# Kernel tuning notes

Hardware: AMD Instinct MI355X
Metric: run time of the kernel (lower is better)

Reference implementation:

```python
import jax, jax.numpy as jnp
import numpy as np

N = 50000   # nodes
E = 800000  # edges
D = 96      # feature dim


def setup_inputs() -> dict:
    key = jax.random.key(0)
    k1, k2, k3, k4 = jax.random.split(key, 4)
    scale = 1.0 / np.sqrt(D)
    return {
        "x": jax.random.normal(k1, (N, D), dtype=jnp.float32),
        "edge_index": jax.random.randint(k2, (2, E), 0, N, dtype=jnp.int64),
        "W1": jax.random.normal(k3, (D, D), dtype=jnp.float32) * scale,
        "b1": jnp.zeros((D,), dtype=jnp.float32),
        "W2": jax.random.normal(k4, (D, D), dtype=jnp.float32) * scale,
        "b2": jnp.zeros((D,), dtype=jnp.float32),
    }


def _gcn_conv(x, src, dst, W, b, n_nodes):
    # PyG GCNConv: linear transform, add self-loops, symmetric normalization,
    # scatter-add aggregation from src (row) to dst (col), then bias.
    h = x @ W  # [N, D_out]
    loops = jnp.arange(n_nodes, dtype=src.dtype)
    s = jnp.concatenate([src, loops])  # [E+N]
    d = jnp.concatenate([dst, loops])  # [E+N]
    deg = jax.ops.segment_sum(jnp.ones_like(d, dtype=h.dtype), d, num_segments=n_nodes)
    dinv = jnp.where(deg > 0, jax.lax.rsqrt(deg), 0.0)  # deg^-1/2, 0 for isolated
    norm = dinv[s] * dinv[d]  # [E+N]
    msg = norm[:, None] * h[s]  # gather + scale
    out = jax.ops.segment_sum(msg, d, num_segments=n_nodes)  # scatter-add
    return out + b


def reference(x, edge_index, W1, b1, W2, b2):
    src, dst = edge_index[0], edge_index[1]
    # dropout p=0.0 -> identity. ReLU after every layer (loop break never fires).
    h = _gcn_conv(x, src, dst, W1, b1, N)
    h = jax.nn.relu(h)
    h = _gcn_conv(h, src, dst, W2, b2, N)
    h = jax.nn.relu(h)
    return h
```

## Files before the change

kernel.cpp:

```cpp
#include <hip/hip_runtime.h>
#include <hip/hip_fp16.h>

#define NN 50000
#define EE 800000
#define DD 96

#define NBIN 196
#define CE   4096
#define CB   196
#define EPT2 16
#define DB   64



__global__ __launch_bounds__(256) void k_hist(const int* __restrict__ ei,
                                              int* __restrict__ histB) {
    __shared__ int hist[NBIN];
    int t = threadIdx.x;
    if (t < NBIN) hist[t] = 0;
    __syncthreads();
    int e0 = blockIdx.x * CE;
#pragma unroll
    for (int k = 0; k < EPT2; ++k) {
        int e = e0 + k * 256 + t;
        if (e < EE) atomicAdd(&hist[ei[EE + e] >> 8], 1);
    }
    __syncthreads();
    if (t < NBIN) histB[t * CB + blockIdx.x] = hist[t];
}


__global__ __launch_bounds__(256) void k_scan_bins(int* __restrict__ histB,
                                                   int* __restrict__ binTot) {
    __shared__ int sh[256];
    int t = threadIdx.x;
    int b = blockIdx.x;
    int v = (t < CB) ? histB[b * CB + t] : 0;
    sh[t] = v;
    __syncthreads();
    for (int off = 1; off < 256; off <<= 1) {
        int u = (t >= off) ? sh[t - off] : 0;
        __syncthreads();
        sh[t] += u;
        __syncthreads();
    }
    if (t < CB) histB[b * CB + t] = sh[t] - v;
    if (t == 255) binTot[b] = sh[255];
}


__global__ __launch_bounds__(256) void k_scan_tot(const int* __restrict__ binTot,
                                                  int* __restrict__ binbase) {
    __shared__ int sh[256];
    int t = threadIdx.x;
    int v = (t < NBIN) ? binTot[t] : 0;
    sh[t] = v;
    __syncthreads();
    for (int off = 1; off < 256; off <<= 1) {
        int u = (t >= off) ? sh[t - off] : 0;
        __syncthreads();
        sh[t] += u;
        __syncthreads();
    }
    if (t < NBIN) binbase[t] = sh[t] - v;
    if (t == 0) binbase[NBIN] = EE;
}


__global__ __launch_bounds__(64) void k_scan_tot64(const int* __restrict__ binTotD,
                                                   int* __restrict__ degBase) {
    __shared__ int sh[DB];
    int t = threadIdx.x;
    int v = binTotD[t];
    sh[t] = v;
    __syncthreads();
    for (int off = 1; off < DB; off <<= 1) {
        int u = (t >= off) ? sh[t - off] : 0;
        __syncthreads();
        sh[t] += u;
        __syncthreads();
    }
    degBase[t] = sh[t] - v;
}


__global__ __launch_bounds__(256) void k_scatter_bins(const int* __restrict__ ei,
                                                      const int* __restrict__ histB,
                                                      const int* __restrict__ binbase,
                                                      int* __restrict__ packed) {
    __shared__ int hist[NBIN];
    __shared__ int lofs[NBIN + 1];
    __shared__ int cur[NBIN];
    __shared__ int sstart[NBIN];
    __shared__ int buf[CE];
    __shared__ int sh[256];
    int t = threadIdx.x;
    int e0 = blockIdx.x * CE;
    int nE = min(CE, EE - e0);

    int s[EPT2], d[EPT2];
#pragma unroll
    for (int k = 0; k < EPT2; ++k) {
        int e = e0 + k * 256 + t;
        s[k] = (e < EE) ? ei[e] : 0;
        d[k] = (e < EE) ? ei[EE + e] : -1;
    }
    if (t < NBIN) hist[t] = 0;
    __syncthreads();
#pragma unroll
    for (int k = 0; k < EPT2; ++k)
        if (d[k] >= 0) atomicAdd(&hist[d[k] >> 8], 1);
    __syncthreads();
    int v = (t < NBIN) ? hist[t] : 0;
    sh[t] = v;
    __syncthreads();
    for (int off = 1; off < 256; off <<= 1) {
        int u = (t >= off) ? sh[t - off] : 0;
        __syncthreads();
        sh[t] += u;
        __syncthreads();
    }
    if (t < NBIN) { lofs[t] = sh[t] - v; cur[t] = sh[t] - v; }
    if (t == 0) lofs[NBIN] = nE;
    if (t < NBIN) sstart[t] = binbase[t] + histB[t * CB + blockIdx.x];
    __syncthreads();
#pragma unroll
    for (int k = 0; k < EPT2; ++k)
        if (d[k] >= 0) {
            int b = d[k] >> 8;
            int pos = atomicAdd(&cur[b], 1);
            buf[pos] = s[k] | ((d[k] & 0xFF) << 16);
        }
    __syncthreads();
    for (int i = t; i < nE; i += 256) {
        int blo = 0, bhi = NBIN;
        while (bhi - blo > 1) {
            int mid = (blo + bhi) >> 1;
            if (lofs[mid] <= i) blo = mid; else bhi = mid;
        }
        packed[sstart[blo] + (i - lofs[blo])] = buf[i];
    }
}


__global__ __launch_bounds__(256) void k_csr(const int* __restrict__ packed,
                                             const int* __restrict__ binbase,
                                             int* __restrict__ rp,
                                             float* __restrict__ dinv,
                                             int* __restrict__ col,
                                             const float* __restrict__ x,
                                             __half* __restrict__ xh,
                                             int* __restrict__ histD) {
    __shared__ int h256[256];
    __shared__ int cur[256];
    __shared__ int sh[256];
    __shared__ float sdinv[256];
    __shared__ int hd[DB];
    int t = threadIdx.x;
    int b = blockIdx.x;
    int base = binbase[b];
    int nE = binbase[b + 1] - base;

    h256[t] = 0;
    if (t < DB) hd[t] = 0;
    __syncthreads();
    for (int i = t; i < nE; i += 256)
        atomicAdd(&h256[(packed[base + i] >> 16) & 0xFF], 1);
    __syncthreads();
    int v = h256[t];
    sh[t] = v;
    __syncthreads();
    for (int off = 1; off < 256; off <<= 1) {
        int u = (t >= off) ? sh[t - off] : 0;
        __syncthreads();
        sh[t] += u;
        __syncthreads();
    }
    int ex = sh[t] - v;
    cur[t] = ex;
    float di = rsqrtf((float)(v + 1));
    sdinv[t] = di;
    int node = b * 256 + t;
    if (node <= NN) rp[node] = base + ex;
    if (node < NN) {
        dinv[node] = di;
        atomicAdd(&hd[(DB - 1) - min(v, DB - 1)], 1);
    }
    __syncthreads();
    if (t < DB) histD[t * CB + b] = hd[t];
    for (int i = t; i < nE; i += 256) {
        int pv = packed[base + i];
        int pos = atomicAdd(&cur[(pv >> 16) & 0xFF], 1);
        col[base + pos] = pv & 0xFFFF;
    }
    for (int i = t; i < 256 * 12; i += 256) {
        int rr = i / 12;
        int cc = i % 12;
        int r = b * 256 + rr;
        if (r < NN) {
            float sc = sdinv[rr];
            const float4* xx = (const float4*)x + (size_t)r * 24 + cc * 2;
            float4 f0 = xx[0], f1 = xx[1];
            __half h[8];
            h[0] = __float2half_rn(sc * f0.x); h[1] = __float2half_rn(sc * f0.y);
            h[2] = __float2half_rn(sc * f0.z); h[3] = __float2half_rn(sc * f0.w);
            h[4] = __float2half_rn(sc * f1.x); h[5] = __float2half_rn(sc * f1.y);
            h[6] = __float2half_rn(sc * f1.z); h[7] = __float2half_rn(sc * f1.w);
            ((uint4*)xh)[(size_t)r * 12 + cc] = *(uint4*)h;
        }
    }
}


__global__ __launch_bounds__(256) void k_perm(const int* __restrict__ rp,
                                              const int* __restrict__ histD,
                                              const int* __restrict__ degBase,
                                              int* __restrict__ perm) {
    __shared__ int lcur[DB];
    int t = threadIdx.x;
    int b = blockIdx.x;
    if (t < DB) lcur[t] = 0;
    __syncthreads();
    int node = b * 256 + t;
    if (node < NN) {
        int deg = rp[node + 1] - rp[node];
        int bin = (DB - 1) - min(deg, DB - 1);
        int loc = atomicAdd(&lcur[bin], 1);
        perm[degBase[bin] + histD[bin * CB + b] + loc] = node;
    }
}


template <int FINAL>
__global__ __launch_bounds__(384) void k_fused(const __half* __restrict__ xh,
                                               const int* __restrict__ rp,
                                               const int* __restrict__ col,
                                               const float* __restrict__ dinv,
                                               const int* __restrict__ perm,
                                               const float* __restrict__ W,
                                               const float* __restrict__ b,
                                               __half* __restrict__ acth,
                                               float* __restrict__ outf) {
    __shared__ __half Wl[DD * DD];
    __shared__ float Al[32][100];
    int t = threadIdx.x;
    for (int i = t; i < DD * DD / 8; i += 384) {
        const float4* ww = (const float4*)W;
        float4 f0 = ww[i * 2], f1 = ww[i * 2 + 1];
        __half h[8];
        h[0] = __float2half_rn(f0.x); h[1] = __float2half_rn(f0.y);
        h[2] = __float2half_rn(f0.z); h[3] = __float2half_rn(f0.w);
        h[4] = __float2half_rn(f1.x); h[5] = __float2half_rn(f1.y);
        h[6] = __float2half_rn(f1.z); h[7] = __float2half_rn(f1.w);
        ((uint4*)Wl)[i] = *(uint4*)h;
    }

    int c  = t % 12;
    int ny = t / 12;
    int idx = blockIdx.x * 32 + ny;
    int d = (idx < NN) ? perm[idx] : NN;
    const uint4* h4 = (const uint4*)xh;

    if (d < NN) {
        union U { uint4 u; __half2 h[4]; };
        U self; self.u = h4[d * 12 + c];
        float dd = dinv[d];
        int j0 = rp[d], j1 = rp[d + 1];

        float2 aA[4] = {{0,0},{0,0},{0,0},{0,0}};
        float2 aB[4] = {{0,0},{0,0},{0,0},{0,0}};
        int j = j0;
        for (; j + 3 < j1; j += 4) {
            int s0 = col[j], s1 = col[j+1], s2 = col[j+2], s3 = col[j+3];
            U v0, v1, v2, v3;
            v0.u = h4[s0 * 12 + c];
            v1.u = h4[s1 * 12 + c];
            v2.u = h4[s2 * 12 + c];
            v3.u = h4[s3 * 12 + c];
#pragma unroll
            for (int k = 0; k < 4; ++k) {
                float2 f0 = __half22float2(v0.h[k]);
                float2 f1 = __half22float2(v1.h[k]);
                float2 f2 = __half22float2(v2.h[k]);
                float2 f3 = __half22float2(v3.h[k]);
                aA[k].x += f0.x + f1.x; aA[k].y += f0.y + f1.y;
                aB[k].x += f2.x + f3.x; aB[k].y += f2.y + f3.y;
            }
        }
        for (; j < j1; ++j) {
            U v; v.u = h4[col[j] * 12 + c];
#pragma unroll
            for (int k = 0; k < 4; ++k) {
                float2 f = __half22float2(v.h[k]);
                aA[k].x += f.x; aA[k].y += f.y;
            }
        }
        float v[8];
#pragma unroll
        for (int k = 0; k < 4; ++k) {
            float2 fs = __half22float2(self.h[k]);
            v[2*k]   = dd * (aA[k].x + aB[k].x + fs.x);
            v[2*k+1] = dd * (aA[k].y + aB[k].y + fs.y);
        }
        *(float4*)&Al[ny][c * 8]     = make_float4(v[0], v[1], v[2], v[3]);
        *(float4*)&Al[ny][c * 8 + 4] = make_float4(v[4], v[5], v[6], v[7]);
    }
    __syncthreads();

    int tx = t % 24;
    int ry = t / 24;
    int c0 = tx * 4;
    float a0x = 0.f, a0y = 0.f, a0z = 0.f, a0w = 0.f;
    float a1x = 0.f, a1y = 0.f, a1z = 0.f, a1w = 0.f;
#pragma unroll 8
    for (int k = 0; k < DD; ++k) {
        uint2 wv = *(const uint2*)&Wl[k * DD + c0];
        const __half2* wh = (const __half2*)&wv;
        float2 w01 = __half22float2(wh[0]);
        float2 w23 = __half22float2(wh[1]);
        float r0 = Al[ry][k];
        float r1 = Al[ry + 16][k];
        a0x += r0 * w01.x; a0y += r0 * w01.y; a0z += r0 * w23.x; a0w += r0 * w23.y;
        a1x += r1 * w01.x; a1y += r1 * w01.y; a1z += r1 * w23.x; a1w += r1 * w23.y;
    }
    float4 bb = *(const float4*)&b[c0];
    int i0 = blockIdx.x * 32 + ry;
    int i1 = i0 + 16;
    int g0 = (i0 < NN) ? perm[i0] : NN;
    int g1 = (i1 < NN) ? perm[i1] : NN;
    float r0x = fmaxf(a0x + bb.x, 0.f), r0y = fmaxf(a0y + bb.y, 0.f);
    float r0z = fmaxf(a0z + bb.z, 0.f), r0w = fmaxf(a0w + bb.w, 0.f);
    float r1x = fmaxf(a1x + bb.x, 0.f), r1y = fmaxf(a1y + bb.y, 0.f);
    float r1z = fmaxf(a1z + bb.z, 0.f), r1w = fmaxf(a1w + bb.w, 0.f);
    if (g0 < NN) {
        if (FINAL) {
            *(float4*)&outf[g0 * DD + c0] = make_float4(r0x, r0y, r0z, r0w);
        } else {
            float sc = dinv[g0];
            __half h[4];
            h[0] = __float2half_rn(sc * r0x); h[1] = __float2half_rn(sc * r0y);
            h[2] = __float2half_rn(sc * r0z); h[3] = __float2half_rn(sc * r0w);
            *(uint2*)&acth[g0 * DD + c0] = *(uint2*)h;
        }
    }
    if (g1 < NN) {
        if (FINAL) {
            *(float4*)&outf[g1 * DD + c0] = make_float4(r1x, r1y, r1z, r1w);
        } else {
            float sc = dinv[g1];
            __half h[4];
            h[0] = __float2half_rn(sc * r1x); h[1] = __float2half_rn(sc * r1y);
            h[2] = __float2half_rn(sc * r1z); h[3] = __float2half_rn(sc * r1w);
            *(uint2*)&acth[g1 * DD + c0] = *(uint2*)h;
        }
    }
}


extern "C" void kernel_launch(void* const* d_in, const int* in_sizes, int n_in,
                              void* d_out, int out_size, void* d_ws, size_t ws_size,
                              hipStream_t stream) {
    const float* x  = (const float*)d_in[0];
    const int*   ei = (const int*)d_in[1];
    const float* W1 = (const float*)d_in[2];
    const float* b1 = (const float*)d_in[3];
    const float* W2 = (const float*)d_in[4];
    const float* b2 = (const float*)d_in[5];
    float* out = (float*)d_out;

    char* p = (char*)d_ws;
    int*   histB   = (int*)p;   p += ((size_t)NBIN * CB * 4 + 255) & ~(size_t)255;
    int*   binTot  = (int*)p;   p += ((size_t)NBIN * 4 + 255) & ~(size_t)255;
    int*   binbase = (int*)p;   p += ((size_t)(NBIN + 1) * 4 + 255) & ~(size_t)255;
    int*   rp      = (int*)p;   p += ((size_t)(NN + 1) * 4 + 255) & ~(size_t)255;
    float* dinv    = (float*)p; p += ((size_t)NN * 4 + 255) & ~(size_t)255;
    int*   col     = (int*)p;   p += ((size_t)EE * 4 + 255) & ~(size_t)255;
    int*   histD   = (int*)p;   p += ((size_t)DB * CB * 4 + 255) & ~(size_t)255;
    int*   binTotD = (int*)p;   p += ((size_t)DB * 4 + 255) & ~(size_t)255;
    int*   degBase = (int*)p;   p += ((size_t)DB * 4 + 255) & ~(size_t)255;
    int*   perm    = (int*)p;   p += ((size_t)NN * 4 + 255) & ~(size_t)255;
    __half* bufA   = (__half*)p; p += ((size_t)NN * DD * 2 + 255) & ~(size_t)255;
    __half* bufB   = (__half*)p;
    int*   packed  = (int*)bufB;

    k_hist<<<CB, 256, 0, stream>>>(ei, histB);
    k_scan_bins<<<NBIN, 256, 0, stream>>>(histB, binTot);
    k_scan_tot<<<1, 256, 0, stream>>>(binTot, binbase);
    k_scatter_bins<<<CB, 256, 0, stream>>>(ei, histB, binbase, packed);
    k_csr<<<NBIN, 256, 0, stream>>>(packed, binbase, rp, dinv, col, x, bufA, histD);
    k_scan_bins<<<DB, 256, 0, stream>>>(histD, binTotD);
    k_scan_tot64<<<1, 64, 0, stream>>>(binTotD, degBase);
    k_perm<<<NBIN, 256, 0, stream>>>(rp, histD, degBase, perm);

    k_fused<0><<<(NN + 31) / 32, 384, 0, stream>>>(bufA, rp, col, dinv, perm,
                                                   W1, b1, bufB, nullptr);

    k_fused<1><<<(NN + 31) / 32, 384, 0, stream>>>(bufB, rp, col, dinv, perm,
                                                   W2, b2, nullptr, out);
}
```

Before: 137.4 us.

## Fold bin scans into consumers and build a block-local degree permutation inside k_csr

The two single-block scan kernels are removed. Each block of k_scatter_bins and k_csr now recomputes the exclusive prefix sum over the per-bin totals in shared memory itself. The global degree-sorted permutation (histD, its scans and k_perm) is replaced by sorting nodes by degree only within each 256-node bin inside k_csr. This cuts the launch count from eight to four preprocessing kernels and shortens the serial dependency chain. The cost is some redundant scan work per block and a weaker, block-local degree ordering for load balancing in the fused aggregation kernels.

```diff
diff --git a/kernel.cpp b/kernel.cpp
--- a/kernel.cpp
+++ b/kernel.cpp
@@ -49,44 +49,9 @@
 }
 
 
-__global__ __launch_bounds__(256) void k_scan_tot(const int* __restrict__ binTot,
-                                                  int* __restrict__ binbase) {
-    __shared__ int sh[256];
-    int t = threadIdx.x;
-    int v = (t < NBIN) ? binTot[t] : 0;
-    sh[t] = v;
-    __syncthreads();
-    for (int off = 1; off < 256; off <<= 1) {
-        int u = (t >= off) ? sh[t - off] : 0;
-        __syncthreads();
-        sh[t] += u;
-        __syncthreads();
-    }
-    if (t < NBIN) binbase[t] = sh[t] - v;
-    if (t == 0) binbase[NBIN] = EE;
-}
-
-
-__global__ __launch_bounds__(64) void k_scan_tot64(const int* __restrict__ binTotD,
-                                                   int* __restrict__ degBase) {
-    __shared__ int sh[DB];
-    int t = threadIdx.x;
-    int v = binTotD[t];
-    sh[t] = v;
-    __syncthreads();
-    for (int off = 1; off < DB; off <<= 1) {
-        int u = (t >= off) ? sh[t - off] : 0;
-        __syncthreads();
-        sh[t] += u;
-        __syncthreads();
-    }
-    degBase[t] = sh[t] - v;
-}
-
-
 __global__ __launch_bounds__(256) void k_scatter_bins(const int* __restrict__ ei,
                                                       const int* __restrict__ histB,
-                                                      const int* __restrict__ binbase,
+                                                      const int* __restrict__ binTot,
                                                       int* __restrict__ packed) {
     __shared__ int hist[NBIN];
     __shared__ int lofs[NBIN + 1];
@@ -105,6 +70,18 @@
         s[k] = (e < EE) ? ei[e] : 0;
         d[k] = (e < EE) ? ei[EE + e] : -1;
     }
+    int bt = (t < NBIN) ? binTot[t] : 0;
+    sh[t] = bt;
+    __syncthreads();
+    for (int off = 1; off < 256; off <<= 1) {
+        int u = (t >= off) ? sh[t - off] : 0;
+        __syncthreads();
+        sh[t] += u;
+        __syncthreads();
+    }
+    int mybinbase = sh[t] - bt;
+    __syncthreads();
+
     if (t < NBIN) hist[t] = 0;
     __syncthreads();
 #pragma unroll
@@ -122,7 +99,7 @@
     }
     if (t < NBIN) { lofs[t] = sh[t] - v; cur[t] = sh[t] - v; }
     if (t == 0) lofs[NBIN] = nE;
-    if (t < NBIN) sstart[t] = binbase[t] + histB[t * CB + blockIdx.x];
+    if (t < NBIN) sstart[t] = mybinbase + histB[t * CB + blockIdx.x];
     __syncthreads();
 #pragma unroll
     for (int k = 0; k < EPT2; ++k)
@@ -144,25 +121,39 @@
 
 
 __global__ __launch_bounds__(256) void k_csr(const int* __restrict__ packed,
-                                             const int* __restrict__ binbase,
+                                             const int* __restrict__ binTot,
                                              int* __restrict__ rp,
                                              float* __restrict__ dinv,
                                              int* __restrict__ col,
                                              const float* __restrict__ x,
                                              __half* __restrict__ xh,
-                                             int* __restrict__ histD) {
+                                             int* __restrict__ perm) {
     __shared__ int h256[256];
     __shared__ int cur[256];
     __shared__ int sh[256];
     __shared__ float sdinv[256];
-    __shared__ int hd[DB];
+    __shared__ int hdBase[DB];
+    __shared__ int hdCur[DB];
+    __shared__ int s_base, s_n;
     int t = threadIdx.x;
     int b = blockIdx.x;
-    int base = binbase[b];
-    int nE = binbase[b + 1] - base;
+
+    int bt = (t < NBIN) ? binTot[t] : 0;
+    sh[t] = bt;
+    __syncthreads();
+    for (int off = 1; off < 256; off <<= 1) {
+        int u = (t >= off) ? sh[t - off] : 0;
+        __syncthreads();
+        sh[t] += u;
+        __syncthreads();
+    }
+    if (t == b) { s_base = sh[t] - bt; s_n = bt; }
+    __syncthreads();
+    int base = s_base;
+    int nE = s_n;
 
     h256[t] = 0;
-    if (t < DB) hd[t] = 0;
+    if (t < DB) hdCur[t] = 0;
     __syncthreads();
     for (int i = t; i < nE; i += 256)
         atomicAdd(&h256[(packed[base + i] >> 16) & 0xFF], 1);
@@ -182,12 +173,30 @@
     sdinv[t] = di;
     int node = b * 256 + t;
     if (node <= NN) rp[node] = base + ex;
+    if (node < NN) dinv[node] = di;
+    __syncthreads();
+
+    int db = (DB - 1) - min(v, DB - 1);
+    h256[t] = 0;
+    __syncthreads();
+    if (node < NN) atomicAdd(&h256[db], 1);
+    __syncthreads();
+    int hv = (t < DB) ? h256[t] : 0;
+    sh[t] = hv;
+    __syncthreads();
+    for (int off = 1; off < 256; off <<= 1) {
+        int u = (t >= off) ? sh[t - off] : 0;
+        __syncthreads();
+        sh[t] += u;
+        __syncthreads();
+    }
+    if (t < DB) hdBase[t] = sh[t] - hv;
+    __syncthreads();
     if (node < NN) {
-        dinv[node] = di;
-        atomicAdd(&hd[(DB - 1) - min(v, DB - 1)], 1);
-    }
-    __syncthreads();
-    if (t < DB) histD[t * CB + b] = hd[t];
+        int rank = hdBase[db] + atomicAdd(&hdCur[db], 1);
+        perm[b * 256 + rank] = node;
+    }
+
     for (int i = t; i < nE; i += 256) {
         int pv = packed[base + i];
         int pos = atomicAdd(&cur[(pv >> 16) & 0xFF], 1);
@@ -208,25 +217,6 @@
             h[6] = __float2half_rn(sc * f1.z); h[7] = __float2half_rn(sc * f1.w);
             ((uint4*)xh)[(size_t)r * 12 + cc] = *(uint4*)h;
         }
-    }
-}
-
-
-__global__ __launch_bounds__(256) void k_perm(const int* __restrict__ rp,
-                                              const int* __restrict__ histD,
-                                              const int* __restrict__ degBase,
-                                              int* __restrict__ perm) {
-    __shared__ int lcur[DB];
-    int t = threadIdx.x;
-    int b = blockIdx.x;
-    if (t < DB) lcur[t] = 0;
-    __syncthreads();
-    int node = b * 256 + t;
-    if (node < NN) {
-        int deg = rp[node + 1] - rp[node];
-        int bin = (DB - 1) - min(deg, DB - 1);
-        int loc = atomicAdd(&lcur[bin], 1);
-        perm[degBase[bin] + histD[bin * CB + b] + loc] = node;
     }
 }
 
@@ -371,13 +361,9 @@
     char* p = (char*)d_ws;
     int*   histB   = (int*)p;   p += ((size_t)NBIN * CB * 4 + 255) & ~(size_t)255;
     int*   binTot  = (int*)p;   p += ((size_t)NBIN * 4 + 255) & ~(size_t)255;
-    int*   binbase = (int*)p;   p += ((size_t)(NBIN + 1) * 4 + 255) & ~(size_t)255;
     int*   rp      = (int*)p;   p += ((size_t)(NN + 1) * 4 + 255) & ~(size_t)255;
     float* dinv    = (float*)p; p += ((size_t)NN * 4 + 255) & ~(size_t)255;
     int*   col     = (int*)p;   p += ((size_t)EE * 4 + 255) & ~(size_t)255;
-    int*   histD   = (int*)p;   p += ((size_t)DB * CB * 4 + 255) & ~(size_t)255;
-    int*   binTotD = (int*)p;   p += ((size_t)DB * 4 + 255) & ~(size_t)255;
-    int*   degBase = (int*)p;   p += ((size_t)DB * 4 + 255) & ~(size_t)255;
     int*   perm    = (int*)p;   p += ((size_t)NN * 4 + 255) & ~(size_t)255;
     __half* bufA   = (__half*)p; p += ((size_t)NN * DD * 2 + 255) & ~(size_t)255;
     __half* bufB   = (__half*)p;
@@ -385,12 +371,8 @@
 
     k_hist<<<CB, 256, 0, stream>>>(ei, histB);
     k_scan_bins<<<NBIN, 256, 0, stream>>>(histB, binTot);
-    k_scan_tot<<<1, 256, 0, stream>>>(binTot, binbase);
-    k_scatter_bins<<<CB, 256, 0, stream>>>(ei, histB, binbase, packed);
-    k_csr<<<NBIN, 256, 0, stream>>>(packed, binbase, rp, dinv, col, x, bufA, histD);
-    k_scan_bins<<<DB, 256, 0, stream>>>(histD, binTotD);
-    k_scan_tot64<<<1, 64, 0, stream>>>(binTotD, degBase);
-    k_perm<<<NBIN, 256, 0, stream>>>(rp, histD, degBase, perm);
+    k_scatter_bins<<<CB, 256, 0, stream>>>(ei, histB, binTot, packed);
+    k_csr<<<NBIN, 256, 0, stream>>>(packed, binTot, rp, dinv, col, x, bufA, perm);
 
     k_fused<0><<<(NN + 31) / 32, 384, 0, stream>>>(bufA, rp, col, dinv, perm,
                                                    W1, b1, bufB, nullptr);
```

Measured after the change: 143.3 us. 4.3% more time.
